# Optimization experiments

Measured on AMD Instinct MI355X. Metric: run time of the kernel, lower is better.

Reference implementation:

```python
import jax, jax.numpy as jnp
import numpy as np

B = 100        # number of queries
N = 50000      # n_node
E = 600000     # n_edges
D = 128        # in_dim = out_dim (hidden_dim)
A = 64         # attn_dim
R = 200        # n_rel -> rela_embed has 2*R+1 = 401 rows


def setup_inputs() -> dict:
    key = jax.random.key(0)
    ks = jax.random.split(key, 14)
    q_sub = jax.random.randint(ks[0], (B,), 0, N)
    q_rel = jax.random.randint(ks[1], (B,), 0, 2 * R + 1)
    # edges: [E, 6]; col0=r_idx(<B), col2=rel(<2R+1), col4=sub(<N), col5=obj(<N); cols 1,3 unused
    c0 = jax.random.randint(ks[2], (E,), 0, B)
    c2 = jax.random.randint(ks[3], (E,), 0, 2 * R + 1)
    c4 = jax.random.randint(ks[4], (E,), 0, N)
    c5 = jax.random.randint(ks[5], (E,), 0, N)
    z = jnp.zeros((E,), dtype=jnp.int32)
    edges = jnp.stack([c0, z, c2, z, c4, c5], axis=1)
    hidden = jax.random.normal(ks[6], (N, D), dtype=jnp.float32)
    # learned parameters
    rela_embed = jax.random.normal(ks[7], (2 * R + 1, D), dtype=jnp.float32) * 0.02
    Ws = jax.random.normal(ks[8], (D, A), dtype=jnp.float32) * 0.05   # Ws_attn.weight^T
    Wr = jax.random.normal(ks[9], (D, A), dtype=jnp.float32) * 0.05   # Wr_attn.weight^T
    Wqr = jax.random.normal(ks[10], (D, A), dtype=jnp.float32) * 0.05 # Wqr_attn.weight^T
    bqr = jnp.zeros((A,), dtype=jnp.float32)
    wa = jax.random.normal(ks[11], (A, 1), dtype=jnp.float32) * 0.05  # w_alpha.weight^T
    ba = jnp.zeros((1,), dtype=jnp.float32)
    Wh = jax.random.normal(ks[12], (D, D), dtype=jnp.float32) * 0.05  # W_h.weight^T
    return {"q_sub": q_sub, "q_rel": q_rel, "hidden": hidden, "edges": edges,
            "n_node": N, "rela_embed": rela_embed, "Ws": Ws, "Wr": Wr,
            "Wqr": Wqr, "bqr": bqr, "wa": wa, "ba": ba, "Wh": Wh}


def reference(q_sub, q_rel, hidden, edges, n_node, rela_embed, Ws, Wr, Wqr, bqr, wa, ba, Wh):
    sub = edges[:, 4]
    rel = edges[:, 2]
    obj = edges[:, 5]
    r_idx = edges[:, 0]
    hs = hidden[sub]                       # [E, D] gather
    hr = rela_embed[rel]                   # [E, D] gather
    h_qr = rela_embed[q_rel][r_idx]        # [B, D] then gather -> [E, D]
    # attention score per edge
    pre = hs @ Ws + hr @ Wr + h_qr @ Wqr + bqr          # [E, A]
    alpha = jax.nn.sigmoid(jax.nn.relu(pre) @ wa + ba)   # [E, 1]
    message = alpha * (hs + hr)                          # [E, D]
    message_agg = jax.ops.segment_sum(message, obj, num_segments=n_node)  # [N, D]
    hidden_new = message_agg @ Wh                        # act = identity ('idd')
    return hidden_new
```

## Files before the change

### kernel.cpp

```cpp
#include <hip/hip_runtime.h>

#define DD 128
#define AA 64
#define SS 96

static inline int idiv_up(int a, int b) { return (a + b - 1) / b; }

__device__ __forceinline__ unsigned short f2bf(float f) {
    unsigned u = __float_as_uint(f);
    u += 0x7fff + ((u >> 16) & 1);
    return (unsigned short)(u >> 16);
}
__device__ __forceinline__ float bf2f(unsigned short h) {
    return __uint_as_float(((unsigned)h) << 16);
}

__global__ __launch_bounds__(256)
void proj_hist_kernel(const float* __restrict__ hidden,
                      const float* __restrict__ rela,
                      const int* __restrict__ q_rel,
                      const float* __restrict__ Ws,
                      const float* __restrict__ Wr,
                      const float* __restrict__ Wqr,
                      const float* __restrict__ bqr,
                      const float* __restrict__ Wh,
                      const int* __restrict__ edges,
                      int* __restrict__ deg,
                      float* __restrict__ subrows,
                      float* __restrict__ hrWr,
                      float* __restrict__ relaWh,
                      float* __restrict__ hqrWqr,
                      int N, int NR, int B, int E,
                      int nA, int nB, int nC) {
    __shared__ float lht[128 * 64];
    __shared__ float wslice[128 * 64];
    const int t = threadIdx.x;
    const int bid = blockIdx.x;
    const int nP = 3 * nA + 3 * nB + nC;

    if (bid >= nP) {
        const int base = (bid - nP) * 4096;
        #pragma unroll
        for (int k = 0; k < 4; ++k) {
            const int e0 = base + (k * 256 + t) * 4;
            if (e0 >= E) break;
            if (e0 + 3 < E) {
                const int4* p = (const int4*)&edges[(long)e0 * 6];
                const int4 j1 = p[1], j2 = p[2], j4 = p[4], j5 = p[5];
                atomicAdd(&deg[j1.y], 1);
                atomicAdd(&deg[j2.w], 1);
                atomicAdd(&deg[j4.y], 1);
                atomicAdd(&deg[j5.w], 1);
            } else {
                for (int e = e0; e < E; ++e) atomicAdd(&deg[edges[(long)e * 6 + 5]], 1);
            }
        }
        return;
    }

    int type, tile, s, nrows;
    const float* src;
    if (bid < 3 * nA)           { type = 0; tile = bid / 3;            s = bid - tile * 3;       nrows = N;  src = hidden; }
    else if (bid < 3 * (nA+nB)) { const int pb = bid - 3 * nA; type = 1; tile = pb / 3; s = pb - tile * 3; nrows = NR; src = rela; }
    else                        { type = 2; tile = bid - 3 * (nA+nB);  s = 0;                    nrows = B;  src = rela; }
    const int rbase = tile * 64;

    const float* W;
    int ldw, off;
    if (s == 0) { W = (type == 0) ? Ws : (type == 1) ? Wr : Wqr; ldw = 64;  off = 0; }
    else if (s == 1) { W = Wh; ldw = 128; off = 0; }
    else             { W = Wh; ldw = 128; off = 64; }

    #pragma unroll
    for (int k = 0; k < 8192; k += 1024) {
        const int f = k + t * 4;
        *(float4*)&wslice[f] = *(const float4*)&W[(long)(f >> 6) * ldw + off + (f & 63)];
    }

    const int row = t & 63;
    const int d0 = (t >> 6) * 32;
    const int gr = rbase + row;
    const float* srow = nullptr;
    if (gr < nrows) {
        const int sr = (type == 2) ? q_rel[gr] : gr;
        srow = src + (long)sr * DD;
    }
    #pragma unroll
    for (int j = 0; j < 8; ++j) {
        float4 v = make_float4(0.f, 0.f, 0.f, 0.f);
        if (srow) v = *(const float4*)&srow[d0 + j * 4];
        lht[(d0 + j * 4 + 0) * 64 + row] = v.x;
        lht[(d0 + j * 4 + 1) * 64 + row] = v.y;
        lht[(d0 + j * 4 + 2) * 64 + row] = v.z;
        lht[(d0 + j * 4 + 3) * 64 + row] = v.w;
    }
    __syncthreads();

    const int r0 = (t & 15) * 4;
    const int c0 = (t >> 4) * 4;

    float acc[4][4] = {};
    #pragma unroll 4
    for (int d = 0; d < 128; ++d) {
        const float4 hv = *(const float4*)&lht[d * 64 + r0];
        const float4 wv = *(const float4*)&wslice[d * 64 + c0];
        acc[0][0] = fmaf(hv.x, wv.x, acc[0][0]);
        acc[0][1] = fmaf(hv.x, wv.y, acc[0][1]);
        acc[0][2] = fmaf(hv.x, wv.z, acc[0][2]);
        acc[0][3] = fmaf(hv.x, wv.w, acc[0][3]);
        acc[1][0] = fmaf(hv.y, wv.x, acc[1][0]);
        acc[1][1] = fmaf(hv.y, wv.y, acc[1][1]);
        acc[1][2] = fmaf(hv.y, wv.z, acc[1][2]);
        acc[1][3] = fmaf(hv.y, wv.w, acc[1][3]);
        acc[2][0] = fmaf(hv.z, wv.x, acc[2][0]);
        acc[2][1] = fmaf(hv.z, wv.y, acc[2][1]);
        acc[2][2] = fmaf(hv.z, wv.z, acc[2][2]);
        acc[2][3] = fmaf(hv.z, wv.w, acc[2][3]);
        acc[3][0] = fmaf(hv.w, wv.x, acc[3][0]);
        acc[3][1] = fmaf(hv.w, wv.y, acc[3][1]);
        acc[3][2] = fmaf(hv.w, wv.z, acc[3][2]);
        acc[3][3] = fmaf(hv.w, wv.w, acc[3][3]);
    }

    #pragma unroll
    for (int i = 0; i < 4; ++i) {
        const int orow = rbase + r0 + i;
        if (orow >= nrows) continue;
        if (type == 0) {
            float* srw = subrows + (long)orow * SS;
            ushort4 o;
            o.x = f2bf(acc[i][0]); o.y = f2bf(acc[i][1]);
            o.z = f2bf(acc[i][2]); o.w = f2bf(acc[i][3]);
            if (s == 0)      *(ushort4*)((unsigned short*)srw + c0) = o;
            else if (s == 1) *(ushort4*)((unsigned short*)(srw + 32) + c0) = o;
            else             *(ushort4*)((unsigned short*)(srw + 32) + 64 + c0) = o;
        } else if (type == 1) {
            const float4 o = make_float4(acc[i][0], acc[i][1], acc[i][2], acc[i][3]);
            if (s == 0)      *(float4*)&hrWr[(long)orow * 64 + c0] = o;
            else if (s == 1) *(float4*)&relaWh[(long)orow * 128 + c0] = o;
            else             *(float4*)&relaWh[(long)orow * 128 + 64 + c0] = o;
        } else {
            const float4 bq = *(const float4*)&bqr[c0];
            *(float4*)&hqrWqr[(long)orow * 64 + c0] =
                make_float4(acc[i][0] + bq.x, acc[i][1] + bq.y,
                            acc[i][2] + bq.z, acc[i][3] + bq.w);
        }
    }
}

__global__ __launch_bounds__(256)
void scan_kernel(const int* __restrict__ deg, int* __restrict__ loff,
                 int* __restrict__ cur, int* __restrict__ bsum,
                 int* __restrict__ bsumx, int* __restrict__ done,
                 int n, int nb) {
    __shared__ int tsum[256];
    __shared__ int lastFlag;
    const int t = threadIdx.x;
    const int b = blockIdx.x;
    const int base = b * 1024 + t * 4;
    int v[4];
    int s = 0;
    #pragma unroll
    for (int j = 0; j < 4; ++j) {
        v[j] = (base + j < n) ? deg[base + j] : 0;
        s += v[j];
    }
    tsum[t] = s;
    __syncthreads();
    for (int o = 1; o < 256; o <<= 1) {
        const int x = (t >= o) ? tsum[t - o] : 0;
        __syncthreads();
        tsum[t] += x;
        __syncthreads();
    }
    int run = (t > 0) ? tsum[t - 1] : 0;
    #pragma unroll
    for (int j = 0; j < 4; ++j) {
        if (base + j < n) { loff[base + j] = run; cur[base + j] = run; }
        run += v[j];
    }
    if (t == 255) {
        bsum[b] = tsum[255];
        __threadfence();
    }
    __syncthreads();
    if (t == 0) lastFlag = (atomicAdd(done, 1) == nb - 1);
    __syncthreads();
    if (lastFlag && t < 64) {
        __threadfence();
        const int val = (t < nb) ? bsum[t] : 0;
        int inc = val;
        #pragma unroll
        for (int o = 1; o < 64; o <<= 1) {
            const int x = __shfl_up(inc, o, 64);
            if (t >= o) inc += x;
        }
        if (t < nb) bsumx[t] = inc - val;
    }
}

__global__ void scatter_kernel(const int* __restrict__ edges, int* cur,
                               const int* __restrict__ bsumx,
                               int2* __restrict__ recs, int E) {
    const int e0 = (blockIdx.x * blockDim.x + threadIdx.x) * 4;
    if (e0 >= E) return;
    if (e0 + 3 < E) {
        const int4* p = (const int4*)&edges[(long)e0 * 6];
        const int4 j0 = p[0], j1 = p[1], j2 = p[2], j3 = p[3], j4 = p[4], j5 = p[5];
        {
            const int pos = bsumx[j1.y >> 10] + atomicAdd(&cur[j1.y], 1);
            recs[pos] = make_int2(j1.x, j0.z | (j0.x << 16));
        }
        {
            const int pos = bsumx[j2.w >> 10] + atomicAdd(&cur[j2.w], 1);
            recs[pos] = make_int2(j2.z, j2.x | (j1.z << 16));
        }
        {
            const int pos = bsumx[j4.y >> 10] + atomicAdd(&cur[j4.y], 1);
            recs[pos] = make_int2(j4.x, j3.z | (j3.x << 16));
        }
        {
            const int pos = bsumx[j5.w >> 10] + atomicAdd(&cur[j5.w], 1);
            recs[pos] = make_int2(j5.z, j5.x | (j4.z << 16));
        }
    } else {
        for (int e = e0; e < E; ++e) {
            const int* ed = edges + (long)e * 6;
            const int obj = ed[5];
            const int pos = bsumx[obj >> 10] + atomicAdd(&cur[obj], 1);
            recs[pos] = make_int2(ed[4], ed[2] | (ed[0] << 16));
        }
    }
}

__global__ __launch_bounds__(256)
void gather_kernel(const int2* __restrict__ recs,
                   const int* __restrict__ loff,
                   const int* __restrict__ bsumx,
                   const float* __restrict__ subrows,
                   const float* __restrict__ hrWr,
                   const float* __restrict__ hqrWqr,
                   const float* __restrict__ relaWh,
                   const float* __restrict__ wa,
                   const float* __restrict__ ba,
                   float* __restrict__ out, int N, int E) {
    const int lane = threadIdx.x & 63;
    const int g = lane >> 4;
    const int l = lane & 15;
    const int v = (int)((blockIdx.x * blockDim.x + threadIdx.x) >> 6);
    if (v >= N) return;
    const float4 wav = *(const float4*)&wa[l * 4];
    const float bar = ba[0];
    const int start = loff[v] + bsumx[v >> 10];
    const int end = (v + 1 < N) ? (loff[v + 1] + bsumx[(v + 1) >> 10]) : E;

    float4 acc0 = make_float4(0.f, 0.f, 0.f, 0.f);
    float4 acc1 = make_float4(0.f, 0.f, 0.f, 0.f);

    for (int base = start; base < end; base += 8) {
        const int k1 = base + g;
        const int k2 = base + 4 + g;
        const bool va1 = (k1 < end);
        const bool va2 = (k2 < end);
        const int2 rc1 = va1 ? recs[k1] : make_int2(0, 0);
        const int2 rc2 = va2 ? recs[k2] : make_int2(0, 0);
        const int sub1 = rc1.x, rel1 = rc1.y & 0xffff, rid1 = rc1.y >> 16;
        const int sub2 = rc2.x, rel2 = rc2.y & 0xffff, rid2 = rc2.y >> 16;
        const float* sr1 = subrows + (long)sub1 * SS;
        const float* sr2 = subrows + (long)sub2 * SS;

        const ushort4 hw1 = *(const ushort4*)((const unsigned short*)sr1 + l * 4);
        const ushort4 hw2 = *(const ushort4*)((const unsigned short*)sr2 + l * 4);
        const float4 b41 = *(const float4*)&hrWr[rel1 * AA + l * 4];
        const float4 b42 = *(const float4*)&hrWr[rel2 * AA + l * 4];
        const float4 c41 = *(const float4*)&hqrWqr[rid1 * AA + l * 4];
        const float4 c42 = *(const float4*)&hqrWqr[rid2 * AA + l * 4];
        const ushort4 m01 = *(const ushort4*)((const unsigned short*)(sr1 + 32) + l * 8);
        const ushort4 m11 = *(const ushort4*)((const unsigned short*)(sr1 + 32) + l * 8 + 4);
        const ushort4 m02 = *(const ushort4*)((const unsigned short*)(sr2 + 32) + l * 8);
        const ushort4 m12 = *(const ushort4*)((const unsigned short*)(sr2 + 32) + l * 8 + 4);
        const float4 r01 = *(const float4*)&relaWh[rel1 * DD + l * 8];
        const float4 r11 = *(const float4*)&relaWh[rel1 * DD + l * 8 + 4];
        const float4 r02 = *(const float4*)&relaWh[rel2 * DD + l * 8];
        const float4 r12 = *(const float4*)&relaWh[rel2 * DD + l * 8 + 4];

        float s1 = fmaxf(bf2f(hw1.x) + b41.x + c41.x, 0.f) * wav.x;
        s1 = fmaf(fmaxf(bf2f(hw1.y) + b41.y + c41.y, 0.f), wav.y, s1);
        s1 = fmaf(fmaxf(bf2f(hw1.z) + b41.z + c41.z, 0.f), wav.z, s1);
        s1 = fmaf(fmaxf(bf2f(hw1.w) + b41.w + c41.w, 0.f), wav.w, s1);
        float s2 = fmaxf(bf2f(hw2.x) + b42.x + c42.x, 0.f) * wav.x;
        s2 = fmaf(fmaxf(bf2f(hw2.y) + b42.y + c42.y, 0.f), wav.y, s2);
        s2 = fmaf(fmaxf(bf2f(hw2.z) + b42.z + c42.z, 0.f), wav.z, s2);
        s2 = fmaf(fmaxf(bf2f(hw2.w) + b42.w + c42.w, 0.f), wav.w, s2);
        s1 += __shfl_xor(s1, 1);  s2 += __shfl_xor(s2, 1);
        s1 += __shfl_xor(s1, 2);  s2 += __shfl_xor(s2, 2);
        s1 += __shfl_xor(s1, 4);  s2 += __shfl_xor(s2, 4);
        s1 += __shfl_xor(s1, 8);  s2 += __shfl_xor(s2, 8);
        float al1 = __builtin_amdgcn_rcpf(1.0f + __expf(-(s1 + bar)));
        float al2 = __builtin_amdgcn_rcpf(1.0f + __expf(-(s2 + bar)));
        if (!va1) al1 = 0.0f;
        if (!va2) al2 = 0.0f;

        acc0.x = fmaf(al1, bf2f(m01.x) + r01.x, acc0.x);
        acc0.y = fmaf(al1, bf2f(m01.y) + r01.y, acc0.y);
        acc0.z = fmaf(al1, bf2f(m01.z) + r01.z, acc0.z);
        acc0.w = fmaf(al1, bf2f(m01.w) + r01.w, acc0.w);
        acc1.x = fmaf(al1, bf2f(m11.x) + r11.x, acc1.x);
        acc1.y = fmaf(al1, bf2f(m11.y) + r11.y, acc1.y);
        acc1.z = fmaf(al1, bf2f(m11.z) + r11.z, acc1.z);
        acc1.w = fmaf(al1, bf2f(m11.w) + r11.w, acc1.w);
        acc0.x = fmaf(al2, bf2f(m02.x) + r02.x, acc0.x);
        acc0.y = fmaf(al2, bf2f(m02.y) + r02.y, acc0.y);
        acc0.z = fmaf(al2, bf2f(m02.z) + r02.z, acc0.z);
        acc0.w = fmaf(al2, bf2f(m02.w) + r02.w, acc0.w);
        acc1.x = fmaf(al2, bf2f(m12.x) + r12.x, acc1.x);
        acc1.y = fmaf(al2, bf2f(m12.y) + r12.y, acc1.y);
        acc1.z = fmaf(al2, bf2f(m12.z) + r12.z, acc1.z);
        acc1.w = fmaf(al2, bf2f(m12.w) + r12.w, acc1.w);
    }

    #pragma unroll
    for (int o = 16; o <= 32; o <<= 1) {
        acc0.x += __shfl_xor(acc0.x, o);
        acc0.y += __shfl_xor(acc0.y, o);
        acc0.z += __shfl_xor(acc0.z, o);
        acc0.w += __shfl_xor(acc0.w, o);
        acc1.x += __shfl_xor(acc1.x, o);
        acc1.y += __shfl_xor(acc1.y, o);
        acc1.z += __shfl_xor(acc1.z, o);
        acc1.w += __shfl_xor(acc1.w, o);
    }
    if (g == 0) {
        *(float4*)&out[(long)v * DD + l * 8]     = acc0;
        *(float4*)&out[(long)v * DD + l * 8 + 4] = acc1;
    }
}

extern "C" void kernel_launch(void* const* d_in, const int* in_sizes, int n_in,
                              void* d_out, int out_size, void* d_ws, size_t ws_size,
                              hipStream_t stream) {
    const int*   q_rel  = (const int*)d_in[1];
    const float* hidden = (const float*)d_in[2];
    const int*   edges  = (const int*)d_in[3];
    const float* rela   = (const float*)d_in[5];
    const float* Ws     = (const float*)d_in[6];
    const float* Wr     = (const float*)d_in[7];
    const float* Wqr    = (const float*)d_in[8];
    const float* bqr    = (const float*)d_in[9];
    const float* wa     = (const float*)d_in[10];
    const float* ba     = (const float*)d_in[11];
    const float* Wh     = (const float*)d_in[12];

    const int B  = in_sizes[1];
    const int N  = in_sizes[2] / DD;
    const int E  = in_sizes[3] / 6;
    const int NR = in_sizes[5] / DD;

    float* out = (float*)d_out;

    float* subrows = (float*)d_ws;
    float* hrWr    = subrows + (size_t)N * SS;
    float* relaWh  = hrWr + (size_t)NR * AA;
    float* hqrWqr  = relaWh + (size_t)NR * DD;
    int*   deg     = (int*)(hqrWqr + (size_t)B * AA);
    int*   done    = deg + N;
    int*   cur     = done + 3;
    int*   loff    = cur + N;
    int*   bsum    = loff + N;
    int*   bsumx   = bsum + 64;
    int2*  recs    = (int2*)(bsumx + 64);

    const int nA = idiv_up(N, 64);
    const int nB = idiv_up(NR, 64);
    const int nC = idiv_up(B, 64);
    const int nH = idiv_up(E, 4096);
    const int nb = idiv_up(N, 1024);
    const int grid_ph = 3 * nA + 3 * nB + nC + nH;

    hipMemsetAsync(deg, 0, (size_t)(N + 1) * sizeof(int), stream);
    proj_hist_kernel<<<grid_ph, 256, 0, stream>>>(
        hidden, rela, q_rel, Ws, Wr, Wqr, bqr, Wh, edges, deg,
        subrows, hrWr, relaWh, hqrWqr, N, NR, B, E, nA, nB, nC);
    scan_kernel<<<nb, 256, 0, stream>>>(deg, loff, cur, bsum, bsumx, done, N, nb);
    scatter_kernel<<<idiv_up(E, 1024), 256, 0, stream>>>(edges, cur, bsumx, recs, E);
    gather_kernel<<<idiv_up(N * 64, 256), 256, 0, stream>>>(
        recs, loff, bsumx, subrows, hrWr, hqrWqr, relaWh, wa, ba, out, N, E);
}
```

Measured before the change: 257.2 us.

## Restructure projection GEMM to one block per row tile with wave-uniform weight reads

The projection kernel previously ran three blocks per 64-row tile, each staging a 128x64 weight slice and the transposed input tile in LDS. Now one 192-thread block loads the input tile once into padded LDS, and each wave computes 64 output columns for one row per lane. Weights are read directly from global memory with wave-uniform addresses, so they can be served as scalar loads. This removes the duplicate input-tile loads and the weight staging, at the cost of 64 accumulator registers per thread and lower occupancy. The histogram part is resized to match the new block size.

After: 268.1 us. 1.04x slower.

```diff
diff --git a/kernel.cpp b/kernel.cpp
--- a/kernel.cpp
+++ b/kernel.cpp
@@ -3,6 +3,8 @@
 #define DD 128
 #define AA 64
 #define SS 96
+#define PB 192
+#define RP 132
 
 static inline int idiv_up(int a, int b) { return (a + b - 1) / b; }
 
@@ -15,7 +17,7 @@
     return __uint_as_float(((unsigned)h) << 16);
 }
 
-__global__ __launch_bounds__(256)
+__global__ __launch_bounds__(PB)
 void proj_hist_kernel(const float* __restrict__ hidden,
                       const float* __restrict__ rela,
                       const int* __restrict__ q_rel,
@@ -32,17 +34,16 @@
                       float* __restrict__ hqrWqr,
                       int N, int NR, int B, int E,
                       int nA, int nB, int nC) {
-    __shared__ float lht[128 * 64];
-    __shared__ float wslice[128 * 64];
+    __shared__ float lht[64 * RP];
     const int t = threadIdx.x;
     const int bid = blockIdx.x;
-    const int nP = 3 * nA + 3 * nB + nC;
+    const int nP = nA + nB + nC;
 
     if (bid >= nP) {
-        const int base = (bid - nP) * 4096;
+        const int base = (bid - nP) * 3072;
         #pragma unroll
         for (int k = 0; k < 4; ++k) {
-            const int e0 = base + (k * 256 + t) * 4;
+            const int e0 = base + (k * PB + t) * 4;
             if (e0 >= E) break;
             if (e0 + 3 < E) {
                 const int4* p = (const int4*)&edges[(long)e0 * 6];
@@ -58,92 +59,90 @@
         return;
     }
 
-    int type, tile, s, nrows;
+    int type, tile, nrows;
     const float* src;
-    if (bid < 3 * nA)           { type = 0; tile = bid / 3;            s = bid - tile * 3;       nrows = N;  src = hidden; }
-    else if (bid < 3 * (nA+nB)) { const int pb = bid - 3 * nA; type = 1; tile = pb / 3; s = pb - tile * 3; nrows = NR; src = rela; }
-    else                        { type = 2; tile = bid - 3 * (nA+nB);  s = 0;                    nrows = B;  src = rela; }
+    if (bid < nA)           { type = 0; tile = bid;           nrows = N;  src = hidden; }
+    else if (bid < nA + nB) { type = 1; tile = bid - nA;      nrows = NR; src = rela; }
+    else                    { type = 2; tile = bid - nA - nB; nrows = B;  src = rela; }
     const int rbase = tile * 64;
 
+    for (int f = t * 4; f < 8192; f += PB * 4) {
+        const int row = f >> 7;
+        const int col = f & 127;
+        float4 v = make_float4(0.f, 0.f, 0.f, 0.f);
+        const int gr = rbase + row;
+        if (gr < nrows) {
+            const int sr = (type == 2) ? q_rel[gr] : gr;
+            v = *(const float4*)&src[(long)sr * DD + col];
+        }
+        *(float4*)&lht[row * RP + col] = v;
+    }
+    __syncthreads();
+
+    const int lane = t & 63;
+    const int wid = __builtin_amdgcn_readfirstlane(t >> 6);
+
     const float* W;
-    int ldw, off;
-    if (s == 0) { W = (type == 0) ? Ws : (type == 1) ? Wr : Wqr; ldw = 64;  off = 0; }
-    else if (s == 1) { W = Wh; ldw = 128; off = 0; }
-    else             { W = Wh; ldw = 128; off = 64; }
-
+    int ldw, coff;
+    if (wid == 0) {
+        W = (type == 0) ? Ws : (type == 1) ? Wr : Wqr;
+        ldw = 64; coff = 0;
+    } else {
+        W = Wh; ldw = 128; coff = (wid == 2) ? 64 : 0;
+    }
+    const float* wbase = W + coff;
+
+    float acc[64];
     #pragma unroll
-    for (int k = 0; k < 8192; k += 1024) {
-        const int f = k + t * 4;
-        *(float4*)&wslice[f] = *(const float4*)&W[(long)(f >> 6) * ldw + off + (f & 63)];
-    }
-
-    const int row = t & 63;
-    const int d0 = (t >> 6) * 32;
-    const int gr = rbase + row;
-    const float* srow = nullptr;
-    if (gr < nrows) {
-        const int sr = (type == 2) ? q_rel[gr] : gr;
-        srow = src + (long)sr * DD;
-    }
-    #pragma unroll
-    for (int j = 0; j < 8; ++j) {
-        float4 v = make_float4(0.f, 0.f, 0.f, 0.f);
-        if (srow) v = *(const float4*)&srow[d0 + j * 4];
-        lht[(d0 + j * 4 + 0) * 64 + row] = v.x;
-        lht[(d0 + j * 4 + 1) * 64 + row] = v.y;
-        lht[(d0 + j * 4 + 2) * 64 + row] = v.z;
-        lht[(d0 + j * 4 + 3) * 64 + row] = v.w;
-    }
-    __syncthreads();
-
-    const int r0 = (t & 15) * 4;
-    const int c0 = (t >> 4) * 4;
-
-    float acc[4][4] = {};
-    #pragma unroll 4
-    for (int d = 0; d < 128; ++d) {
-        const float4 hv = *(const float4*)&lht[d * 64 + r0];
-        const float4 wv = *(const float4*)&wslice[d * 64 + c0];
-        acc[0][0] = fmaf(hv.x, wv.x, acc[0][0]);
-        acc[0][1] = fmaf(hv.x, wv.y, acc[0][1]);
-        acc[0][2] = fmaf(hv.x, wv.z, acc[0][2]);
-        acc[0][3] = fmaf(hv.x, wv.w, acc[0][3]);
-        acc[1][0] = fmaf(hv.y, wv.x, acc[1][0]);
-        acc[1][1] = fmaf(hv.y, wv.y, acc[1][1]);
-        acc[1][2] = fmaf(hv.y, wv.z, acc[1][2]);
-        acc[1][3] = fmaf(hv.y, wv.w, acc[1][3]);
-        acc[2][0] = fmaf(hv.z, wv.x, acc[2][0]);
-        acc[2][1] = fmaf(hv.z, wv.y, acc[2][1]);
-        acc[2][2] = fmaf(hv.z, wv.z, acc[2][2]);
-        acc[2][3] = fmaf(hv.z, wv.w, acc[2][3]);
-        acc[3][0] = fmaf(hv.w, wv.x, acc[3][0]);
-        acc[3][1] = fmaf(hv.w, wv.y, acc[3][1]);
-        acc[3][2] = fmaf(hv.w, wv.z, acc[3][2]);
-        acc[3][3] = fmaf(hv.w, wv.w, acc[3][3]);
-    }
-
-    #pragma unroll
-    for (int i = 0; i < 4; ++i) {
-        const int orow = rbase + r0 + i;
-        if (orow >= nrows) continue;
-        if (type == 0) {
-            float* srw = subrows + (long)orow * SS;
+    for (int c = 0; c < 64; ++c) acc[c] = 0.f;
+
+    for (int d = 0; d < 128; d += 4) {
+        const float4 h = *(const float4*)&lht[lane * RP + d];
+        #pragma unroll
+        for (int cc = 0; cc < 64; cc += 16) {
+            #pragma unroll
+            for (int c = 0; c < 16; ++c) {
+                const int col = cc + c;
+                acc[col] = fmaf(h.x, wbase[(d + 0) * ldw + col], acc[col]);
+                acc[col] = fmaf(h.y, wbase[(d + 1) * ldw + col], acc[col]);
+                acc[col] = fmaf(h.z, wbase[(d + 2) * ldw + col], acc[col]);
+                acc[col] = fmaf(h.w, wbase[(d + 3) * ldw + col], acc[col]);
+            }
+        }
+    }
+
+    const int gr = rbase + lane;
+    if (gr >= nrows) return;
+
+    if (type == 0) {
+        unsigned short* dst = (unsigned short*)(subrows + (long)gr * SS) + wid * 64;
+        #pragma unroll
+        for (int k = 0; k < 16; ++k) {
             ushort4 o;
-            o.x = f2bf(acc[i][0]); o.y = f2bf(acc[i][1]);
-            o.z = f2bf(acc[i][2]); o.w = f2bf(acc[i][3]);
-            if (s == 0)      *(ushort4*)((unsigned short*)srw + c0) = o;
-            else if (s == 1) *(ushort4*)((unsigned short*)(srw + 32) + c0) = o;
-            else             *(ushort4*)((unsigned short*)(srw + 32) + 64 + c0) = o;
-        } else if (type == 1) {
-            const float4 o = make_float4(acc[i][0], acc[i][1], acc[i][2], acc[i][3]);
-            if (s == 0)      *(float4*)&hrWr[(long)orow * 64 + c0] = o;
-            else if (s == 1) *(float4*)&relaWh[(long)orow * 128 + c0] = o;
-            else             *(float4*)&relaWh[(long)orow * 128 + 64 + c0] = o;
+            o.x = f2bf(acc[4 * k + 0]); o.y = f2bf(acc[4 * k + 1]);
+            o.z = f2bf(acc[4 * k + 2]); o.w = f2bf(acc[4 * k + 3]);
+            *(ushort4*)&dst[4 * k] = o;
+        }
+    } else if (type == 1) {
+        if (wid == 0) {
+            #pragma unroll
+            for (int k = 0; k < 16; ++k)
+                *(float4*)&hrWr[(long)gr * 64 + 4 * k] =
+                    make_float4(acc[4*k], acc[4*k+1], acc[4*k+2], acc[4*k+3]);
         } else {
-            const float4 bq = *(const float4*)&bqr[c0];
-            *(float4*)&hqrWqr[(long)orow * 64 + c0] =
-                make_float4(acc[i][0] + bq.x, acc[i][1] + bq.y,
-                            acc[i][2] + bq.z, acc[i][3] + bq.w);
+            float* dst = relaWh + (long)gr * 128 + (wid - 1) * 64;
+            #pragma unroll
+            for (int k = 0; k < 16; ++k)
+                *(float4*)&dst[4 * k] =
+                    make_float4(acc[4*k], acc[4*k+1], acc[4*k+2], acc[4*k+3]);
+        }
+    } else if (wid == 0) {
+        #pragma unroll
+        for (int k = 0; k < 16; ++k) {
+            const float4 bq = *(const float4*)&bqr[4 * k];
+            *(float4*)&hqrWqr[(long)gr * 64 + 4 * k] =
+                make_float4(acc[4*k] + bq.x, acc[4*k+1] + bq.y,
+                            acc[4*k+2] + bq.z, acc[4*k+3] + bq.w);
         }
     }
 }
@@ -373,12 +372,12 @@
     const int nA = idiv_up(N, 64);
     const int nB = idiv_up(NR, 64);
     const int nC = idiv_up(B, 64);
-    const int nH = idiv_up(E, 4096);
+    const int nH = idiv_up(E, 3072);
     const int nb = idiv_up(N, 1024);
-    const int grid_ph = 3 * nA + 3 * nB + nC + nH;
+    const int grid_ph = nA + nB + nC + nH;
 
     hipMemsetAsync(deg, 0, (size_t)(N + 1) * sizeof(int), stream);
-    proj_hist_kernel<<<grid_ph, 256, 0, stream>>>(
+    proj_hist_kernel<<<grid_ph, PB, 0, stream>>>(
         hidden, rela, q_rel, Ws, Wr, Wqr, bqr, Wh, edges, deg,
         subrows, hrWr, relaWh, hqrWqr, N, NR, B, E, nA, nB, nC);
     scan_kernel<<<nb, 256, 0, stream>>>(deg, loff, cur, bsum, bsumx, done, N, nb);
```
